# Performance work log

Hardware: AMD Instinct MI355X
Metric: run time of the kernel (lower is better)

Reference implementation:

```python
import jax, jax.numpy as jnp
import numpy as np

D_ATTN = 64

def setup_inputs() -> dict:
    key = jax.random.key(0)
    k1, k2, k3 = jax.random.split(key, 3)
    B, N, d_ffn = 8, 2048, 1536
    x = jax.random.normal(k1, (B, N, d_ffn), dtype=jnp.float32)
    W_qkv = jax.random.normal(k2, (d_ffn, 3 * D_ATTN), dtype=jnp.float32) * (1.0 / np.sqrt(d_ffn))
    b_qkv = jnp.zeros((3 * D_ATTN,), dtype=jnp.float32)
    W_out = jax.random.normal(k3, (D_ATTN, d_ffn // 2), dtype=jnp.float32) * (1.0 / np.sqrt(D_ATTN))
    b_out = jnp.zeros((d_ffn // 2,), dtype=jnp.float32)
    return {"x": x, "W_qkv": W_qkv, "b_qkv": b_qkv, "W_out": W_out, "b_out": b_out}

def reference(x, W_qkv, b_qkv, W_out, b_out):
    # x: [B, N, d_ffn]
    qkv = jnp.einsum('bnd,de->bne', x, W_qkv) + b_qkv  # [B, N, 3*d_attn]
    q, k, v = jnp.split(qkv, 3, axis=-1)               # each [B, N, d_attn]
    scale = 1.0 / jnp.sqrt(jnp.float32(D_ATTN))
    energy = jnp.einsum('bqd,bkd->bqk', q, k) * scale  # [B, N, N]
    attn = jax.nn.softmax(energy, axis=-1)
    out = jnp.einsum('bqk,bkd->bqd', attn, v)          # [B, N, d_attn]
    out = jnp.einsum('bnd,de->bne', out, W_out) + b_out  # [B, N, d_ffn//2]
    return out
```

## Files before the change

kernel.cpp:

```cpp
#include <hip/hip_runtime.h>
#include <hip/hip_bf16.h>


typedef __attribute__((ext_vector_type(8))) short short8;
typedef __attribute__((ext_vector_type(4))) short short4v;
typedef __attribute__((ext_vector_type(4))) float float4v;
typedef __attribute__((ext_vector_type(16))) float float16v;

#define MFMA16(a, b, c) __builtin_amdgcn_mfma_f32_16x16x32_bf16((a), (b), (c), 0, 0, 0)
#define MFMA32(a, b, c) __builtin_amdgcn_mfma_f32_32x32x16_bf16((a), (b), (c), 0, 0, 0)

static __device__ __forceinline__ void plswap(unsigned& a, unsigned& b) {
  asm("v_permlane32_swap_b32 %0, %1" : "+v"(a), "+v"(b));
}

static __device__ __forceinline__ unsigned short f2bf(float x) {
  union { float f; unsigned u; } v; v.f = x;
  return (unsigned short)((v.u + 0x7FFFu + ((v.u >> 16) & 1u)) >> 16);
}
static __device__ __forceinline__ short8 ldg8(const short* p) {
  return *(const short8*)p;
}

__global__ __launch_bounds__(256) void k_prep(
    const float* __restrict__ Wq, const float* __restrict__ Wo,
    short* __restrict__ Wtf, short* __restrict__ WtO) {
  __shared__ float wl[64 * 52];
  __shared__ __align__(16) short tl[64 * 72];
  const int tid = threadIdx.x;
  int id = blockIdx.x;
  if (id < 96) {
    const int kk = id >> 2, w = id & 3;
    const int r = tid >> 2, cq = (tid & 3) * 12;
    const float* sp = Wq + (size_t)(kk * 64 + r) * 192 + w * 48 + cq;
    float4v a = *(const float4v*)(sp);
    float4v b = *(const float4v*)(sp + 4);
    float4v c4 = *(const float4v*)(sp + 8);
    float* dp = wl + r * 52 + cq;
    *(float4v*)(dp) = a; *(float4v*)(dp + 4) = b; *(float4v*)(dp + 8) = c4;
    __syncthreads();
#pragma unroll
    for (int i = 0; i < 2; ++i) {
      const int fid = i * 256 + tid;
      if (fid < 384) {
        const int frag = fid >> 6, lane = fid & 63;
        const int lo = lane & 15, hi = lane >> 4;
        const int c = frag >> 1, ks = frag & 1;
        short8 o;
#pragma unroll
        for (int e = 0; e < 8; ++e)
          o[e] = (short)f2bf(wl[(ks * 32 + hi * 8 + e) * 52 + c * 16 + lo]);
        *(short8*)(Wtf + ((((size_t)kk * 4 + w) * 6 + frag) << 9) + lane * 8) = o;
      }
    }
  } else {
    id -= 96;
    const int r = tid >> 2, cq = (tid & 3) * 16;
    const float* sp = Wo + (size_t)r * 768 + id * 64 + cq;
    float4v v0 = *(const float4v*)(sp);
    float4v v1 = *(const float4v*)(sp + 4);
    float4v v2 = *(const float4v*)(sp + 8);
    float4v v3 = *(const float4v*)(sp + 12);
    short8 s0, s1;
#pragma unroll
    for (int i = 0; i < 4; ++i) {
      s0[i] = (short)f2bf(v0[i]); s0[i + 4] = (short)f2bf(v1[i]);
      s1[i] = (short)f2bf(v2[i]); s1[i + 4] = (short)f2bf(v3[i]);
    }
    *(short8*)(tl + r * 72 + cq) = s0;
    *(short8*)(tl + r * 72 + cq + 8) = s1;
    __syncthreads();
    short8 o0, o1;
#pragma unroll
    for (int j = 0; j < 8; ++j) {
      o0[j] = tl[(cq + j) * 72 + r];
      o1[j] = tl[(cq + 8 + j) * 72 + r];
    }
    short* dp2 = WtO + (size_t)(id * 64 + r) * 64 + cq;
    *(short8*)(dp2) = o0;
    *(short8*)(dp2 + 8) = o1;
  }
}

__global__ __launch_bounds__(256) void k_qkv(
    const float* __restrict__ x, const short* __restrict__ Wtf,
    const float* __restrict__ bq, short* __restrict__ Qf,
    short* __restrict__ Kf, short* __restrict__ Vf) {
  __shared__ __align__(16) short xl[2][32 * 72];
  __shared__ __align__(16) short qbuf[32 * 72], kstg[32 * 72], vstg[32 * 72];
  const int tid = threadIdx.x;
  const int w = tid >> 6, lane = tid & 63, lo = lane & 15, hi = lane >> 4;
  const int m0 = blockIdx.x * 32;
  const float KSC = 0.18033688011112042f;
  const int cb = w * 48;

  float4v acc[2][3];
#pragma unroll
  for (int r = 0; r < 2; ++r)
#pragma unroll
    for (int c = 0; c < 3; ++c) acc[r][c] = (float4v)0.0f;

  const int xr = tid >> 3, xc = (tid & 7) * 8;
  const float* xrow = x + (size_t)(m0 + xr) * 1536 + xc;
  short* xlw0 = &xl[0][xr * 72 + xc];
  short* xlw1 = &xl[1][xr * 72 + xc];

  const short* wbase = Wtf + ((size_t)w * 6) * 512 + lane * 8;

  float4v xv0 = *(const float4v*)(xrow + 0);
  float4v xv1 = *(const float4v*)(xrow + 4);
  short8 bcur[3][2];
#pragma unroll
  for (int c = 0; c < 3; ++c)
#pragma unroll
    for (int ks = 0; ks < 2; ++ks)
      bcur[c][ks] = ldg8(wbase + (c * 2 + ks) * 512);
  {
    short8 s0;
#pragma unroll
    for (int i = 0; i < 4; ++i) { s0[i] = (short)f2bf(xv0[i]); s0[i + 4] = (short)f2bf(xv1[i]); }
    *(short8*)(xlw0) = s0;
  }
  __syncthreads();

  for (int kk = 0; kk < 24; ++kk) {
    const int cur = kk & 1;
    short8 bnxt[3][2];
    if (kk < 23) {
      const int k1 = (kk + 1) * 64;
      xv0 = *(const float4v*)(xrow + k1 + 0);
      xv1 = *(const float4v*)(xrow + k1 + 4);
      const short* wn = wbase + (size_t)(kk + 1) * 12288;
#pragma unroll
      for (int c = 0; c < 3; ++c)
#pragma unroll
        for (int ks = 0; ks < 2; ++ks)
          bnxt[c][ks] = ldg8(wn + (c * 2 + ks) * 512);
    }
    const short* xb = &xl[cur][0];
#pragma unroll
    for (int r = 0; r < 2; ++r) {
      short8 a0 = *(const short8*)(xb + (r * 16 + lo) * 72 + hi * 8);
      short8 a1 = *(const short8*)(xb + (r * 16 + lo) * 72 + 32 + hi * 8);
#pragma unroll
      for (int c = 0; c < 3; ++c) {
        acc[r][c] = MFMA16(a0, bcur[c][0], acc[r][c]);
        acc[r][c] = MFMA16(a1, bcur[c][1], acc[r][c]);
      }
    }
    if (kk < 23) {
      short8 s0;
#pragma unroll
      for (int i = 0; i < 4; ++i) { s0[i] = (short)f2bf(xv0[i]); s0[i + 4] = (short)f2bf(xv1[i]); }
      *(short8*)(cur ? xlw0 : xlw1) = s0;
#pragma unroll
      for (int c = 0; c < 3; ++c) { bcur[c][0] = bnxt[c][0]; bcur[c][1] = bnxt[c][1]; }
    }
    __syncthreads();
  }

  float bb[3];
#pragma unroll
  for (int c = 0; c < 3; ++c) bb[c] = bq[cb + c * 16 + lo];

  const int b = m0 >> 11;
  const int row0 = m0 & 2047;

#pragma unroll
  for (int r = 0; r < 2; ++r)
#pragma unroll
    for (int c = 0; c < 3; ++c) {
      const int colb = cb + c * 16;
      short* buf = (colb < 64) ? qbuf : ((colb < 128) ? kstg : vstg);
      const int d0 = (colb & 63) + lo;
#pragma unroll
      for (int j = 0; j < 4; ++j) {
        float vv = acc[r][c][j] + bb[c];
        if (colb < 64) vv *= KSC;
        buf[(r * 16 + hi * 4 + j) * 72 + d0] = (short)f2bf(vv);
      }
    }
  __syncthreads();

  {
    const int rr = tid >> 3, dq = (tid & 7) * 8;
    const int t32 = row0 >> 5, i = dq >> 4, h = (dq >> 3) & 1;
    const size_t base = ((((size_t)b * 64 + t32) * 4 + i) * 2 + h) * 256 + rr * 8;
    *(short8*)(Qf + base) = *(const short8*)(qbuf + rr * 72 + dq);
    *(short8*)(Kf + base) = *(const short8*)(kstg + rr * 72 + dq);
  }

  {
    const int dr = tid >> 2, kq8 = (tid & 3) * 8;
    short8 o0;
#pragma unroll
    for (int j = 0; j < 8; ++j) o0[j] = vstg[(kq8 + j) * 72 + dr];
    const int kg = row0 >> 5, s = (kq8 >> 4) & 1, h = (kq8 >> 3) & 1;
    const int dc = dr >> 5, c32 = dr & 31;
    short* vp = Vf + ((((((size_t)b * 64 + kg) * 2 + dc) * 2 + s) * 2 + h) * 32 + c32) * 8;
    *(short8*)(vp) = o0;
  }
}

__global__ __launch_bounds__(512) void k_attn(
    const short* __restrict__ Qf, const short* __restrict__ Kf,
    const short* __restrict__ Vf, short* __restrict__ att) {
  __shared__ float Od[8][32][76];
  __shared__ float Ol[8][32];
  const int tid = threadIdx.x;
  const int w = tid >> 6, lane = tid & 63;
  const int c = lane & 31, h = lane >> 5;
  const int b = blockIdx.x >> 6;
  const int qg = blockIdx.x & 63;
  const size_t g0 = (size_t)b * 2048 + qg * 32;

  short8 qf0 = ldg8(Qf + (((size_t)b * 64 + qg) * 4 + 0) * 512 + lane * 8);
  short8 qf1 = ldg8(Qf + (((size_t)b * 64 + qg) * 4 + 1) * 512 + lane * 8);
  short8 qf2 = ldg8(Qf + (((size_t)b * 64 + qg) * 4 + 2) * 512 + lane * 8);
  short8 qf3 = ldg8(Qf + (((size_t)b * 64 + qg) * 4 + 3) * 512 + lane * 8);

  float lp = 0.0f;
  float16v acc0 = (float16v)0.0f;
  float16v acc1 = (float16v)0.0f;

  int kg = w * 8;
  const short* kb = Kf + ((size_t)b * 64) * 2048 + lane * 8;
  const short* vb = Vf + ((size_t)b * 64) * 2048 + lane * 8;

#define ATTN_STEP(K0, K1, K2, K3, V0, V1, V2, V3)                              \
  do {                                                                         \
    float16v sf = (float16v)0.0f;                                              \
    sf = MFMA32(K0, qf0, sf);                                                  \
    sf = MFMA32(K1, qf1, sf);                                                  \
    sf = MFMA32(K2, qf2, sf);                                                  \
    sf = MFMA32(K3, qf3, sf);                                                  \
    unsigned wpk[8];                                                           \
    _Pragma("unroll")                                                          \
    for (int m = 0; m < 8; ++m) {                                              \
      float p0 = __builtin_amdgcn_exp2f(sf[2 * m]);                            \
      float p1 = __builtin_amdgcn_exp2f(sf[2 * m + 1]);                        \
      unsigned u0 = __builtin_bit_cast(unsigned, p0) & 0xFFFF0000u;            \
      unsigned u1 = __builtin_bit_cast(unsigned, p1) & 0xFFFF0000u;            \
      lp += __builtin_bit_cast(float, u0) + __builtin_bit_cast(float, u1);     \
      wpk[m] = (u0 >> 16) | u1;                                                \
    }                                                                          \
    plswap(wpk[0], wpk[2]);                                                    \
    plswap(wpk[1], wpk[3]);                                                    \
    plswap(wpk[4], wpk[6]);                                                    \
    plswap(wpk[5], wpk[7]);                                                    \
    union { unsigned u[4]; short8 s8; } bt0, bt1;                              \
    bt0.u[0] = wpk[0]; bt0.u[1] = wpk[1]; bt0.u[2] = wpk[2]; bt0.u[3] = wpk[3];\
    bt1.u[0] = wpk[4]; bt1.u[1] = wpk[5]; bt1.u[2] = wpk[6]; bt1.u[3] = wpk[7];\
    acc0 = MFMA32(V0, bt0.s8, acc0);                                           \
    acc0 = MFMA32(V1, bt1.s8, acc0);                                           \
    acc1 = MFMA32(V2, bt0.s8, acc1);                                           \
    acc1 = MFMA32(V3, bt1.s8, acc1);                                           \
  } while (0)

  const short* kpA = kb + (size_t)kg * 2048;
  const short* vpA = vb + (size_t)kg * 2048;
  short8 ka0 = ldg8(kpA), ka1 = ldg8(kpA + 512), ka2 = ldg8(kpA + 1024), ka3 = ldg8(kpA + 1536);
  short8 va0 = ldg8(vpA), va1 = ldg8(vpA + 512), va2 = ldg8(vpA + 1024), va3 = ldg8(vpA + 1536);

  for (int t = 0; t < 8; t += 2) {
    const short* kpB = kb + (size_t)(kg + 1) * 2048;
    const short* vpB = vb + (size_t)(kg + 1) * 2048;
    short8 kb0 = ldg8(kpB), kb1 = ldg8(kpB + 512), kb2 = ldg8(kpB + 1024), kb3 = ldg8(kpB + 1536);
    short8 vb0 = ldg8(vpB), vb1 = ldg8(vpB + 512), vb2 = ldg8(vpB + 1024), vb3 = ldg8(vpB + 1536);

    ATTN_STEP(ka0, ka1, ka2, ka3, va0, va1, va2, va3);

    if (t + 2 < 8) {
      const short* kpN = kb + (size_t)(kg + 2) * 2048;
      const short* vpN = vb + (size_t)(kg + 2) * 2048;
      ka0 = ldg8(kpN); ka1 = ldg8(kpN + 512); ka2 = ldg8(kpN + 1024); ka3 = ldg8(kpN + 1536);
      va0 = ldg8(vpN); va1 = ldg8(vpN + 512); va2 = ldg8(vpN + 1024); va3 = ldg8(vpN + 1536);
    }

    ATTN_STEP(kb0, kb1, kb2, kb3, vb0, vb1, vb2, vb3);
    kg += 2;
  }
#undef ATTN_STEP

  lp += __shfl_xor(lp, 32, 64);

#pragma unroll
  for (int g = 0; g < 4; ++g) {
    float4v a0, a1;
#pragma unroll
    for (int r = 0; r < 4; ++r) { a0[r] = acc0[4 * g + r]; a1[r] = acc1[4 * g + r]; }
    *(float4v*)(&Od[w][c][8 * g + 4 * h]) = a0;
    *(float4v*)(&Od[w][c][32 + 8 * g + 4 * h]) = a1;
  }
  if (h == 0) Ol[w][c] = lp;
  __syncthreads();

  {
    const int q = tid >> 4, dq = (tid & 15) * 4;
    float L = 0.0f;
    float4v o = (float4v)0.0f;
#pragma unroll
    for (int w2 = 0; w2 < 8; ++w2) {
      L += Ol[w2][q];
      o += *(const float4v*)(&Od[w2][q][dq]);
    }
    const float inv = 1.0f / L;
    short4v r;
#pragma unroll
    for (int j = 0; j < 4; ++j) r[j] = (short)f2bf(o[j] * inv);
    *(short4v*)(att + (g0 + q) * 64 + dq) = r;
  }
}

__global__ __launch_bounds__(256) void k_out(
    const short* __restrict__ att, const short* __restrict__ WtO,
    const float* __restrict__ bo, float* __restrict__ out) {
  const int tid = threadIdx.x;
  const int w = tid >> 6, lane = tid & 63, lo = lane & 15, hi = lane >> 4;
  const int wc = w * 192;
  const int m0 = blockIdx.x * 32;

  short8 af[2][2];
#pragma unroll
  for (int rf = 0; rf < 2; ++rf) {
    const short* ap = att + (size_t)(m0 + rf * 16 + lo) * 64 + hi * 8;
    af[rf][0] = ldg8(ap);
    af[rf][1] = ldg8(ap + 32);
  }
  float4v acc[2][12];
#pragma unroll
  for (int rf = 0; rf < 2; ++rf)
#pragma unroll
    for (int c = 0; c < 12; ++c) acc[rf][c] = (float4v)0.0f;

#pragma unroll
  for (int c = 0; c < 12; ++c) {
    const short* bp = WtO + (size_t)(wc + c * 16 + lo) * 64 + hi * 8;
    short8 b0 = ldg8(bp);
    short8 b1 = ldg8(bp + 32);
#pragma unroll
    for (int rf = 0; rf < 2; ++rf) {
      acc[rf][c] = MFMA16(af[rf][0], b0, acc[rf][c]);
      acc[rf][c] = MFMA16(af[rf][1], b1, acc[rf][c]);
    }
  }
#pragma unroll
  for (int c = 0; c < 12; ++c) {
    const float bb = bo[wc + c * 16 + lo];
#pragma unroll
    for (int rf = 0; rf < 2; ++rf)
#pragma unroll
      for (int j = 0; j < 4; ++j)
        out[(size_t)(m0 + rf * 16 + hi * 4 + j) * 768 + wc + c * 16 + lo] =
            acc[rf][c][j] + bb;
  }
}

extern "C" void kernel_launch(void* const* d_in, const int* in_sizes, int n_in,
                              void* d_out, int out_size, void* d_ws, size_t ws_size,
                              hipStream_t stream) {
  (void)in_sizes; (void)n_in; (void)out_size; (void)ws_size;
  const float* x  = (const float*)d_in[0];
  const float* Wq = (const float*)d_in[1];
  const float* bq = (const float*)d_in[2];
  const float* Wo = (const float*)d_in[3];
  const float* bo = (const float*)d_in[4];
  float* out = (float*)d_out;

  char* ws = (char*)d_ws;
  short* Qf  = (short*)(ws);
  short* Kf  = (short*)(ws + 2097152);
  short* Vf  = (short*)(ws + 4194304);
  short* att = (short*)(ws + 6291456);
  short* Wtf = (short*)(ws + 8388608);
  short* WtO = (short*)(ws + 8978432);

  k_prep<<<108, 256, 0, stream>>>(Wq, Wo, Wtf, WtO);
  k_qkv<<<512, 256, 0, stream>>>(x, Wtf, bq, Qf, Kf, Vf);
  k_attn<<<512, 512, 0, stream>>>(Qf, Kf, Vf, att);
  k_out<<<512, 256, 0, stream>>>(att, WtO, bo, out);
}
```

Before: 61.91 us.

## Stage x in 384-wide chunks to cut QKV projection barriers

The QKV projection now loads x into shared memory in four 384-column stages with double buffering, where it used 24 stages of 64 columns. Each thread issues 12 float4 loads per stage, and only 4 block barriers remain instead of 24. The aim is more memory-level parallelism and less synchronisation overhead in this memory-bound kernel. In exchange, shared memory grows to about 50KB and register pressure rises from holding 12 float4s, which may reduce occupancy.

```diff
diff --git a/kernel.cpp b/kernel.cpp
--- a/kernel.cpp
+++ b/kernel.cpp
@@ -86,7 +86,7 @@
     const float* __restrict__ x, const short* __restrict__ Wtf,
     const float* __restrict__ bq, short* __restrict__ Qf,
     short* __restrict__ Kf, short* __restrict__ Vf) {
-  __shared__ __align__(16) short xl[2][32 * 72];
+  __shared__ __align__(16) short xs[2][32 * 392];
   __shared__ __align__(16) short qbuf[32 * 72], kstg[32 * 72], vstg[32 * 72];
   const int tid = threadIdx.x;
   const int w = tid >> 6, lane = tid & 63, lo = lane & 15, hi = lane >> 4;
@@ -100,61 +100,71 @@
 #pragma unroll
     for (int c = 0; c < 3; ++c) acc[r][c] = (float4v)0.0f;
 
-  const int xr = tid >> 3, xc = (tid & 7) * 8;
-  const float* xrow = x + (size_t)(m0 + xr) * 1536 + xc;
-  short* xlw0 = &xl[0][xr * 72 + xc];
-  short* xlw1 = &xl[1][xr * 72 + xc];
-
+  const int xr = tid >> 3, g4 = (tid & 7) * 4;
+  const float* xrow = x + (size_t)(m0 + xr) * 1536 + g4;
   const short* wbase = Wtf + ((size_t)w * 6) * 512 + lane * 8;
 
-  float4v xv0 = *(const float4v*)(xrow + 0);
-  float4v xv1 = *(const float4v*)(xrow + 4);
+  float4v xv[12];
+#pragma unroll
+  for (int i = 0; i < 12; ++i) xv[i] = *(const float4v*)(xrow + i * 32);
   short8 bcur[3][2];
 #pragma unroll
   for (int c = 0; c < 3; ++c)
 #pragma unroll
     for (int ks = 0; ks < 2; ++ks)
       bcur[c][ks] = ldg8(wbase + (c * 2 + ks) * 512);
-  {
-    short8 s0;
-#pragma unroll
-    for (int i = 0; i < 4; ++i) { s0[i] = (short)f2bf(xv0[i]); s0[i + 4] = (short)f2bf(xv1[i]); }
-    *(short8*)(xlw0) = s0;
+#pragma unroll
+  for (int i = 0; i < 12; ++i) {
+    short4v sv;
+#pragma unroll
+    for (int j = 0; j < 4; ++j) sv[j] = (short)f2bf(xv[i][j]);
+    *(short4v*)(&xs[0][xr * 392 + g4 + i * 32]) = sv;
   }
   __syncthreads();
 
-  for (int kk = 0; kk < 24; ++kk) {
-    const int cur = kk & 1;
-    short8 bnxt[3][2];
-    if (kk < 23) {
-      const int k1 = (kk + 1) * 64;
-      xv0 = *(const float4v*)(xrow + k1 + 0);
-      xv1 = *(const float4v*)(xrow + k1 + 4);
-      const short* wn = wbase + (size_t)(kk + 1) * 12288;
-#pragma unroll
-      for (int c = 0; c < 3; ++c)
-#pragma unroll
-        for (int ks = 0; ks < 2; ++ks)
-          bnxt[c][ks] = ldg8(wn + (c * 2 + ks) * 512);
-    }
-    const short* xb = &xl[cur][0];
-#pragma unroll
-    for (int r = 0; r < 2; ++r) {
-      short8 a0 = *(const short8*)(xb + (r * 16 + lo) * 72 + hi * 8);
-      short8 a1 = *(const short8*)(xb + (r * 16 + lo) * 72 + 32 + hi * 8);
-#pragma unroll
-      for (int c = 0; c < 3; ++c) {
-        acc[r][c] = MFMA16(a0, bcur[c][0], acc[r][c]);
-        acc[r][c] = MFMA16(a1, bcur[c][1], acc[r][c]);
-      }
-    }
-    if (kk < 23) {
-      short8 s0;
-#pragma unroll
-      for (int i = 0; i < 4; ++i) { s0[i] = (short)f2bf(xv0[i]); s0[i + 4] = (short)f2bf(xv1[i]); }
-      *(short8*)(cur ? xlw0 : xlw1) = s0;
-#pragma unroll
-      for (int c = 0; c < 3; ++c) { bcur[c][0] = bnxt[c][0]; bcur[c][1] = bnxt[c][1]; }
+  int kk = 0;
+  for (int s = 0; s < 4; ++s) {
+    const int cur = s & 1;
+    if (s < 3) {
+#pragma unroll
+      for (int i = 0; i < 12; ++i)
+        xv[i] = *(const float4v*)(xrow + (s + 1) * 384 + i * 32);
+    }
+    const short* xb = &xs[cur][0];
+    for (int kkL = 0; kkL < 6; ++kkL) {
+      short8 bnxt[3][2];
+      if (kk < 23) {
+        const short* wn = wbase + (size_t)(kk + 1) * 12288;
+#pragma unroll
+        for (int c = 0; c < 3; ++c)
+#pragma unroll
+          for (int ks = 0; ks < 2; ++ks)
+            bnxt[c][ks] = ldg8(wn + (c * 2 + ks) * 512);
+      }
+#pragma unroll
+      for (int r = 0; r < 2; ++r) {
+        short8 a0 = *(const short8*)(xb + (r * 16 + lo) * 392 + kkL * 64 + hi * 8);
+        short8 a1 = *(const short8*)(xb + (r * 16 + lo) * 392 + kkL * 64 + 32 + hi * 8);
+#pragma unroll
+        for (int c = 0; c < 3; ++c) {
+          acc[r][c] = MFMA16(a0, bcur[c][0], acc[r][c]);
+          acc[r][c] = MFMA16(a1, bcur[c][1], acc[r][c]);
+        }
+      }
+      if (kk < 23) {
+#pragma unroll
+        for (int c = 0; c < 3; ++c) { bcur[c][0] = bnxt[c][0]; bcur[c][1] = bnxt[c][1]; }
+      }
+      ++kk;
+    }
+    if (s < 3) {
+#pragma unroll
+      for (int i = 0; i < 12; ++i) {
+        short4v sv;
+#pragma unroll
+        for (int j = 0; j < 4; ++j) sv[j] = (short)f2bf(xv[i][j]);
+        *(short4v*)(&xs[cur ^ 1][xr * 392 + g4 + i * 32]) = sv;
+      }
     }
     __syncthreads();
   }
```

After: 66.53 us. 1.07x slower.

## Restructure QKV projection to stage half-K x tiles and 2x2 warp split

Applied to the files above, without the earlier changes.

The QKV projection kernel now converts and stages half of the 32-row x tile (768 columns) into shared memory at once, in two phases, instead of double-buffering 64-column slices with a barrier every step. Each warp now owns 16 rows by 96 output columns (a 2x2 warp grid) rather than all 32 rows by 48 columns. Weight fragments are loaded straight from global memory per K-step, and the launch bound requests 3 blocks per CU. This cuts barriers and is meant to expose more memory-level parallelism, at the cost of larger shared memory and less overlap between weight loads and MFMA.

```diff
diff --git a/kernel.cpp b/kernel.cpp
--- a/kernel.cpp
+++ b/kernel.cpp
@@ -82,104 +82,74 @@
   }
 }
 
-__global__ __launch_bounds__(256) void k_qkv(
+__global__ __launch_bounds__(256, 3) void k_qkv(
     const float* __restrict__ x, const short* __restrict__ Wtf,
     const float* __restrict__ bq, short* __restrict__ Qf,
     short* __restrict__ Kf, short* __restrict__ Vf) {
-  __shared__ __align__(16) short xl[2][32 * 72];
-  __shared__ __align__(16) short qbuf[32 * 72], kstg[32 * 72], vstg[32 * 72];
+  __shared__ __align__(16) short xt[32 * 772];
   const int tid = threadIdx.x;
   const int w = tid >> 6, lane = tid & 63, lo = lane & 15, hi = lane >> 4;
+  const int wr = w >> 1, wc = w & 1;
   const int m0 = blockIdx.x * 32;
   const float KSC = 0.18033688011112042f;
-  const int cb = w * 48;
-
-  float4v acc[2][3];
-#pragma unroll
-  for (int r = 0; r < 2; ++r)
-#pragma unroll
-    for (int c = 0; c < 3; ++c) acc[r][c] = (float4v)0.0f;
-
-  const int xr = tid >> 3, xc = (tid & 7) * 8;
-  const float* xrow = x + (size_t)(m0 + xr) * 1536 + xc;
-  short* xlw0 = &xl[0][xr * 72 + xc];
-  short* xlw1 = &xl[1][xr * 72 + xc];
-
-  const short* wbase = Wtf + ((size_t)w * 6) * 512 + lane * 8;
-
-  float4v xv0 = *(const float4v*)(xrow + 0);
-  float4v xv1 = *(const float4v*)(xrow + 4);
-  short8 bcur[3][2];
-#pragma unroll
-  for (int c = 0; c < 3; ++c)
-#pragma unroll
-    for (int ks = 0; ks < 2; ++ks)
-      bcur[c][ks] = ldg8(wbase + (c * 2 + ks) * 512);
-  {
-    short8 s0;
-#pragma unroll
-    for (int i = 0; i < 4; ++i) { s0[i] = (short)f2bf(xv0[i]); s0[i + 4] = (short)f2bf(xv1[i]); }
-    *(short8*)(xlw0) = s0;
-  }
-  __syncthreads();
-
-  for (int kk = 0; kk < 24; ++kk) {
-    const int cur = kk & 1;
-    short8 bnxt[3][2];
-    if (kk < 23) {
-      const int k1 = (kk + 1) * 64;
-      xv0 = *(const float4v*)(xrow + k1 + 0);
-      xv1 = *(const float4v*)(xrow + k1 + 4);
-      const short* wn = wbase + (size_t)(kk + 1) * 12288;
-#pragma unroll
-      for (int c = 0; c < 3; ++c)
-#pragma unroll
-        for (int ks = 0; ks < 2; ++ks)
-          bnxt[c][ks] = ldg8(wn + (c * 2 + ks) * 512);
-    }
-    const short* xb = &xl[cur][0];
-#pragma unroll
-    for (int r = 0; r < 2; ++r) {
-      short8 a0 = *(const short8*)(xb + (r * 16 + lo) * 72 + hi * 8);
-      short8 a1 = *(const short8*)(xb + (r * 16 + lo) * 72 + 32 + hi * 8);
-#pragma unroll
-      for (int c = 0; c < 3; ++c) {
-        acc[r][c] = MFMA16(a0, bcur[c][0], acc[r][c]);
-        acc[r][c] = MFMA16(a1, bcur[c][1], acc[r][c]);
-      }
-    }
-    if (kk < 23) {
-      short8 s0;
-#pragma unroll
-      for (int i = 0; i < 4; ++i) { s0[i] = (short)f2bf(xv0[i]); s0[i + 4] = (short)f2bf(xv1[i]); }
-      *(short8*)(cur ? xlw0 : xlw1) = s0;
-#pragma unroll
-      for (int c = 0; c < 3; ++c) { bcur[c][0] = bnxt[c][0]; bcur[c][1] = bnxt[c][1]; }
+
+  float4v acc[6];
+#pragma unroll
+  for (int c = 0; c < 6; ++c) acc[c] = (float4v)0.0f;
+
+  const int srow = tid >> 3, scol = (tid & 7) * 4;
+  const float* xrow = x + (size_t)(m0 + srow) * 1536 + scol;
+  short* xw = &xt[srow * 772 + scol];
+
+  for (int ph = 0; ph < 2; ++ph) {
+#pragma unroll
+    for (int i = 0; i < 24; ++i) {
+      float4v v = *(const float4v*)(xrow + ph * 768 + i * 32);
+      short4v sv;
+#pragma unroll
+      for (int j = 0; j < 4; ++j) sv[j] = (short)f2bf(v[j]);
+      *(short4v*)(xw + i * 32) = sv;
     }
     __syncthreads();
-  }
-
-  float bb[3];
-#pragma unroll
-  for (int c = 0; c < 3; ++c) bb[c] = bq[cb + c * 16 + lo];
+
+    const short* xb = &xt[(wr * 16 + lo) * 772 + hi * 8];
+    for (int kkL = 0; kkL < 12; ++kkL) {
+      const int kkG = ph * 12 + kkL;
+      const short* wb = Wtf + ((size_t)(kkG * 4 + wc * 2)) * 3072 + lane * 8;
+      short8 bw[12];
+#pragma unroll
+      for (int f = 0; f < 12; ++f) bw[f] = ldg8(wb + f * 512);
+      short8 a0 = *(const short8*)(xb + kkL * 64);
+      short8 a1 = *(const short8*)(xb + kkL * 64 + 32);
+#pragma unroll
+      for (int f = 0; f < 12; ++f)
+        acc[f >> 1] = MFMA16((f & 1) ? a1 : a0, bw[f], acc[f >> 1]);
+    }
+    __syncthreads();
+  }
+
+  float bb[6];
+#pragma unroll
+  for (int c = 0; c < 6; ++c) bb[c] = bq[wc * 96 + c * 16 + lo];
 
   const int b = m0 >> 11;
   const int row0 = m0 & 2047;
-
-#pragma unroll
-  for (int r = 0; r < 2; ++r)
-#pragma unroll
-    for (int c = 0; c < 3; ++c) {
-      const int colb = cb + c * 16;
-      short* buf = (colb < 64) ? qbuf : ((colb < 128) ? kstg : vstg);
-      const int d0 = (colb & 63) + lo;
-#pragma unroll
-      for (int j = 0; j < 4; ++j) {
-        float vv = acc[r][c][j] + bb[c];
-        if (colb < 64) vv *= KSC;
-        buf[(r * 16 + hi * 4 + j) * 72 + d0] = (short)f2bf(vv);
-      }
-    }
+  short* qbuf = &xt[0];
+  short* kstg = &xt[2304];
+  short* vstg = &xt[4608];
+
+#pragma unroll
+  for (int c = 0; c < 6; ++c) {
+    const int colb = wc * 96 + c * 16;
+    short* buf = (colb < 64) ? qbuf : ((colb < 128) ? kstg : vstg);
+    const int d0 = (colb & 63) + lo;
+#pragma unroll
+    for (int j = 0; j < 4; ++j) {
+      float vv = acc[c][j] + bb[c];
+      if (colb < 64) vv *= KSC;
+      buf[(wr * 16 + hi * 4 + j) * 72 + d0] = (short)f2bf(vv);
+    }
+  }
   __syncthreads();
 
   {
```

New measurement: 78.33 us. 1.27x slower.

## Deepen QKV projection prefetch pipeline to four LDS stages with lighter barriers

Applied to the files above, without the earlier changes.

Rewrites the k_qkv main loop into a 4-stage LDS ring with x loads issued three iterations ahead and weight loads two ahead. This puts more global loads in flight so the projection GEMM hides memory latency better. It also replaces __syncthreads with an explicit lgkmcnt wait plus s_barrier and reuses the ring buffer for the output staging arrays, which lowers LDS use. The cost is higher register pressure and the risk of subtle ordering bugs from the custom barrier.

```diff
diff --git a/kernel.cpp b/kernel.cpp
--- a/kernel.cpp
+++ b/kernel.cpp
@@ -9,6 +9,8 @@
 
 #define MFMA16(a, b, c) __builtin_amdgcn_mfma_f32_16x16x32_bf16((a), (b), (c), 0, 0, 0)
 #define MFMA32(a, b, c) __builtin_amdgcn_mfma_f32_32x32x16_bf16((a), (b), (c), 0, 0, 0)
+
+#define LDS_BARRIER() asm volatile("s_waitcnt lgkmcnt(0)\n\ts_barrier" ::: "memory")
 
 static __device__ __forceinline__ void plswap(unsigned& a, unsigned& b) {
   asm("v_permlane32_swap_b32 %0, %1" : "+v"(a), "+v"(b));
@@ -86,8 +88,7 @@
     const float* __restrict__ x, const short* __restrict__ Wtf,
     const float* __restrict__ bq, short* __restrict__ Qf,
     short* __restrict__ Kf, short* __restrict__ Vf) {
-  __shared__ __align__(16) short xl[2][32 * 72];
-  __shared__ __align__(16) short qbuf[32 * 72], kstg[32 * 72], vstg[32 * 72];
+  __shared__ __align__(16) short xl[4][32 * 72];
   const int tid = threadIdx.x;
   const int w = tid >> 6, lane = tid & 63, lo = lane & 15, hi = lane >> 4;
   const int m0 = blockIdx.x * 32;
@@ -102,62 +103,74 @@
 
   const int xr = tid >> 3, xc = (tid & 7) * 8;
   const float* xrow = x + (size_t)(m0 + xr) * 1536 + xc;
-  short* xlw0 = &xl[0][xr * 72 + xc];
-  short* xlw1 = &xl[1][xr * 72 + xc];
-
+  const int xlo = xr * 72 + xc;
   const short* wbase = Wtf + ((size_t)w * 6) * 512 + lane * 8;
 
-  float4v xv0 = *(const float4v*)(xrow + 0);
-  float4v xv1 = *(const float4v*)(xrow + 4);
-  short8 bcur[3][2];
-#pragma unroll
-  for (int c = 0; c < 3; ++c)
-#pragma unroll
-    for (int ks = 0; ks < 2; ++ks)
-      bcur[c][ks] = ldg8(wbase + (c * 2 + ks) * 512);
-  {
-    short8 s0;
-#pragma unroll
-    for (int i = 0; i < 4; ++i) { s0[i] = (short)f2bf(xv0[i]); s0[i + 4] = (short)f2bf(xv1[i]); }
-    *(short8*)(xlw0) = s0;
-  }
-  __syncthreads();
-
-  for (int kk = 0; kk < 24; ++kk) {
-    const int cur = kk & 1;
-    short8 bnxt[3][2];
-    if (kk < 23) {
-      const int k1 = (kk + 1) * 64;
-      xv0 = *(const float4v*)(xrow + k1 + 0);
-      xv1 = *(const float4v*)(xrow + k1 + 4);
-      const short* wn = wbase + (size_t)(kk + 1) * 12288;
-#pragma unroll
-      for (int c = 0; c < 3; ++c)
-#pragma unroll
-        for (int ks = 0; ks < 2; ++ks)
-          bnxt[c][ks] = ldg8(wn + (c * 2 + ks) * 512);
-    }
-    const short* xb = &xl[cur][0];
-#pragma unroll
-    for (int r = 0; r < 2; ++r) {
-      short8 a0 = *(const short8*)(xb + (r * 16 + lo) * 72 + hi * 8);
-      short8 a1 = *(const short8*)(xb + (r * 16 + lo) * 72 + 32 + hi * 8);
-#pragma unroll
-      for (int c = 0; c < 3; ++c) {
-        acc[r][c] = MFMA16(a0, bcur[c][0], acc[r][c]);
-        acc[r][c] = MFMA16(a1, bcur[c][1], acc[r][c]);
-      }
-    }
-    if (kk < 23) {
-      short8 s0;
-#pragma unroll
-      for (int i = 0; i < 4; ++i) { s0[i] = (short)f2bf(xv0[i]); s0[i + 4] = (short)f2bf(xv1[i]); }
-      *(short8*)(cur ? xlw0 : xlw1) = s0;
-#pragma unroll
-      for (int c = 0; c < 3; ++c) { bcur[c][0] = bnxt[c][0]; bcur[c][1] = bnxt[c][1]; }
-    }
-    __syncthreads();
-  }
+  short8 wA[6], wB[6];
+  float4v xs0[2], xs1[2], xs2[2], xs3[2];
+
+#define ISSUE_X(KK, S)                                                         \
+  do { S[0] = *(const float4v*)(xrow + (KK) * 64);                             \
+       S[1] = *(const float4v*)(xrow + (KK) * 64 + 4); } while (0)
+#define ISSUE_W(KK, WS)                                                        \
+  do { const short* _wp = wbase + (size_t)(KK) * 12288;                        \
+       _Pragma("unroll")                                                       \
+       for (int _f = 0; _f < 6; ++_f) WS[_f] = ldg8(_wp + _f * 512); } while (0)
+#define WRITE_X(S, B)                                                          \
+  do { short8 _sv;                                                             \
+       _Pragma("unroll")                                                       \
+       for (int _j = 0; _j < 4; ++_j) {                                        \
+         _sv[_j] = (short)f2bf(S[0][_j]);                                      \
+         _sv[_j + 4] = (short)f2bf(S[1][_j]);                                  \
+       }                                                                       \
+       *(short8*)(&xl[B][xlo]) = _sv; } while (0)
+#define COMPUTE(B, WS)                                                         \
+  do { const short* _xb = &xl[B][0];                                           \
+       _Pragma("unroll")                                                       \
+       for (int _r = 0; _r < 2; ++_r) {                                        \
+         short8 _a0 = *(const short8*)(_xb + (_r * 16 + lo) * 72 + hi * 8);    \
+         short8 _a1 = *(const short8*)(_xb + (_r * 16 + lo) * 72 + 32 + hi * 8);\
+         _Pragma("unroll")                                                     \
+         for (int _c = 0; _c < 3; ++_c) {                                      \
+           acc[_r][_c] = MFMA16(_a0, WS[2 * _c], acc[_r][_c]);                 \
+           acc[_r][_c] = MFMA16(_a1, WS[2 * _c + 1], acc[_r][_c]);             \
+         }                                                                     \
+       } } while (0)
+
+  ISSUE_X(0, xs0);
+  ISSUE_X(1, xs1);
+  ISSUE_X(2, xs2);
+  ISSUE_W(0, wA);
+  ISSUE_W(1, wB);
+  WRITE_X(xs0, 0);
+  LDS_BARRIER();
+
+  for (int k4 = 0; k4 < 24; k4 += 4) {
+    COMPUTE(0, wA);
+    ISSUE_W(k4 + 2, wA);
+    if (k4 + 3 < 24) ISSUE_X(k4 + 3, xs3);
+    WRITE_X(xs1, 1);
+    LDS_BARRIER();
+    COMPUTE(1, wB);
+    ISSUE_W(k4 + 3, wB);
+    if (k4 + 4 < 24) ISSUE_X(k4 + 4, xs0);
+    WRITE_X(xs2, 2);
+    LDS_BARRIER();
+    COMPUTE(2, wA);
+    if (k4 + 4 < 24) ISSUE_W(k4 + 4, wA);
+    if (k4 + 5 < 24) ISSUE_X(k4 + 5, xs1);
+    if (k4 + 3 < 24) WRITE_X(xs3, 3);
+    LDS_BARRIER();
+    COMPUTE(3, wB);
+    if (k4 + 5 < 24) ISSUE_W(k4 + 5, wB);
+    if (k4 + 6 < 24) ISSUE_X(k4 + 6, xs2);
+    if (k4 + 4 < 24) WRITE_X(xs0, 0);
+    LDS_BARRIER();
+  }
+#undef ISSUE_X
+#undef ISSUE_W
+#undef WRITE_X
+#undef COMPUTE
 
   float bb[3];
 #pragma unroll
@@ -165,6 +178,9 @@
 
   const int b = m0 >> 11;
   const int row0 = m0 & 2047;
+  short* qbuf = &xl[0][0];
+  short* kstg = &xl[1][0];
+  short* vstg = &xl[2][0];
 
 #pragma unroll
   for (int r = 0; r < 2; ++r)
@@ -180,7 +196,7 @@
         buf[(r * 16 + hi * 4 + j) * 72 + d0] = (short)f2bf(vv);
       }
     }
-  __syncthreads();
+  LDS_BARRIER();
 
   {
     const int rr = tid >> 3, dq = (tid & 7) * 8;
```

Result: no change. 62.95 us (+1.7%).
